# Optimization experiments

Hardware: AMD Instinct MI355X
Metric: run time of the kernel (lower is better)

## Reference

```python
import jax, jax.numpy as jnp
import numpy as np

EMBED_DIM = 1024
PROJ_DIM = 512
NUM_HEADS = 8
HEAD_DIM = PROJ_DIM // NUM_HEADS
B, L = 2, 2048


def setup_inputs() -> dict:
    key = jax.random.key(0)
    ks = jax.random.split(key, 7)
    s = lambda d: 1.0 / np.sqrt(d)
    return {
        "x": jax.random.normal(ks[0], (B, L, EMBED_DIM), jnp.float32),
        "proj_W": jax.random.normal(ks[1], (EMBED_DIM, PROJ_DIM), jnp.float32) * s(EMBED_DIM),
        "proj_b": jax.random.normal(ks[2], (PROJ_DIM,), jnp.float32) * 0.01,
        "attn_Wq": jax.random.normal(ks[3], (PROJ_DIM, NUM_HEADS, HEAD_DIM), jnp.float32) * s(PROJ_DIM),
        "attn_Wk": jax.random.normal(ks[4], (PROJ_DIM, NUM_HEADS, HEAD_DIM), jnp.float32) * s(PROJ_DIM),
        "attn_Wv": jax.random.normal(ks[5], (PROJ_DIM, NUM_HEADS, HEAD_DIM), jnp.float32) * s(PROJ_DIM),
        "out_W": jax.random.normal(ks[6], (NUM_HEADS * HEAD_DIM, EMBED_DIM), jnp.float32) * s(NUM_HEADS * HEAD_DIM),
    }


def reference(x, proj_W, proj_b, attn_Wq, attn_Wk, attn_Wv, out_W):
    # ReLU projection: (B, L, embed_dim) -> (B, L, proj_dim)
    p = jax.nn.relu(x @ proj_W + proj_b)
    # Per-head projections: (B, L, C) x (C, H, Dh) -> (B, H, L, Dh)
    q = jnp.einsum('blc,chd->bhld', p, attn_Wq)
    k = jnp.einsum('blc,chd->bhld', p, attn_Wk)
    v = jnp.einsum('blc,chd->bhld', p, attn_Wv)
    scale = 1.0 / np.sqrt(HEAD_DIM).astype(np.float32)
    scores = jnp.einsum('bhqd,bhkd->bhqk', q, k) * scale  # (B, H, L, L)
    weights = jax.nn.softmax(scores, axis=-1)
    heads = jnp.einsum('bhqk,bhkd->bhqd', weights, v)  # (B, H, L, Dh)
    heads = heads.transpose(0, 2, 1, 3).reshape(p.shape[0], p.shape[1], NUM_HEADS * HEAD_DIM)
    return heads @ out_W  # (B, L, embed_dim)
```

## Files before the change

kernel.cpp:

```cpp
#include <hip/hip_runtime.h>
#include <math.h>

#define BATCH 2
#define SEQ 2048
#define BL (BATCH * SEQ)
#define EMBED 1024
#define PROJ 512
#define NHEADS 8
#define HDIM 64
#define QKVN (3 * PROJ)
#define KVSPLIT 4
#define KVQ (SEQ / KVSPLIT)

typedef _Float16 half8 __attribute__((ext_vector_type(8)));
typedef __fp16 fp16x2 __attribute__((ext_vector_type(2)));
typedef float floatx4 __attribute__((ext_vector_type(4)));
typedef float floatx16 __attribute__((ext_vector_type(16)));

__global__ __launch_bounds__(256) void trconv_all(const float* __restrict__ pW,
                                                  const float* __restrict__ Wq,
                                                  const float* __restrict__ Wk,
                                                  const float* __restrict__ Wv,
                                                  const float* __restrict__ oW,
                                                  _Float16* __restrict__ pWt,
                                                  _Float16* __restrict__ qkvWt,
                                                  _Float16* __restrict__ oWt) {
    __shared__ float tile[64][65];
    int id = blockIdx.x;
    const float* src;
    _Float16* dst;
    int K, N;
    float scale = 1.0f;
    if (id < 128)      { src = pW; dst = pWt; K = EMBED; N = PROJ; }
    else if (id < 192) { src = Wq; dst = qkvWt; K = PROJ; N = PROJ;
                         scale = 0.125f * 1.44269504f; id -= 128; }
    else if (id < 256) { src = Wk; dst = qkvWt + (size_t)PROJ * PROJ; K = PROJ; N = PROJ; id -= 192; }
    else if (id < 320) { src = Wv; dst = qkvWt + (size_t)2 * PROJ * PROJ; K = PROJ; N = PROJ; id -= 256; }
    else               { src = oW; dst = oWt; K = PROJ; N = EMBED; id -= 320; }

    const int tn = N / 64;
    const int n0 = (id % tn) * 64;
    const int k0 = (id / tn) * 64;

    const int t  = threadIdx.x;
    const int tx = t & 63;
    const int ty = t >> 6;
#pragma unroll
    for (int i = 0; i < 16; ++i) {
        int k = ty * 16 + i;
        tile[k][tx] = src[(size_t)(k0 + k) * N + n0 + tx];
    }
    __syncthreads();
#pragma unroll
    for (int i = 0; i < 16; ++i) {
        int n = ty * 16 + i;
        dst[(size_t)(n0 + n) * K + k0 + tx] = (_Float16)(tile[tx][n] * scale);
    }
}

__global__ __launch_bounds__(256) void trans_v(const _Float16* __restrict__ v,
                                               _Float16* __restrict__ vt) {
    __shared__ _Float16 tile[64][72];
    const int t  = threadIdx.x;
    const int t0 = blockIdx.x * 64;
    const int h  = blockIdx.y;
    const int b  = blockIdx.z;
    {
        const int r = t >> 2, c0 = (t & 3) * 16;
        const _Float16* src = v + (size_t)(b * SEQ + t0 + r) * QKVN + h * HDIM + c0;
        *reinterpret_cast<half8*>(&tile[r][c0])     = *reinterpret_cast<const half8*>(src);
        *reinterpret_cast<half8*>(&tile[r][c0 + 8]) = *reinterpret_cast<const half8*>(src + 8);
    }
    __syncthreads();
    {
        const int c = t >> 2, k0 = (t & 3) * 16;
        half8 o1, o2;
#pragma unroll
        for (int i = 0; i < 8; ++i) { o1[i] = tile[k0 + i][c]; o2[i] = tile[k0 + 8 + i][c]; }
        _Float16* dst = vt + ((size_t)(b * NHEADS + h) * HDIM + c) * SEQ + t0 + k0;
        *reinterpret_cast<half8*>(dst)     = o1;
        *reinterpret_cast<half8*>(dst + 8) = o2;
    }
}

template <int BM, int BN, int A_F32, int BIASRELU, int C_F32>
__global__ __launch_bounds__(256) void gemm_mfma(const void* __restrict__ Ap,
                                                 const _Float16* __restrict__ Bt,
                                                 const float* __restrict__ bias,
                                                 void* __restrict__ Cp,
                                                 int M, int N, int K) {
    __shared__ _Float16 Ah[BM][40];
    __shared__ _Float16 Bh[BN][40];

    constexpr int MF = BM / 32;
    constexpr int NF = BN / 32;
    constexpr int EPA = BM / 8;
    constexpr int TPA = 32 / EPA;
    constexpr int EPB = BN / 8;
    constexpr int TPB = 32 / EPB;

    const int t  = threadIdx.x;
    const int w  = t >> 6;
    const int l  = t & 63;
    const int lr = l & 15;
    const int lg = l >> 4;
    const int bm = blockIdx.y * BM;
    const int bn = blockIdx.x * BN;
    const int wr = w >> 1;
    const int wc = w & 1;

    const int ar = t / TPA, ac = (t % TPA) * EPA;
    const int br = t / TPB, bc = (t % TPB) * EPB;

    floatx4 acc[MF][NF];
#pragma unroll
    for (int i = 0; i < MF; ++i)
#pragma unroll
        for (int j = 0; j < NF; ++j) acc[i][j] = (floatx4){0.f, 0.f, 0.f, 0.f};

    float4 af[EPA / 4];
    half8  ah[EPA / 8];
    half8  bh[EPB / 8];

    const float* Af = (const float*)Ap;
    const _Float16* Ah16 = (const _Float16*)Ap;

    if (A_F32) {
#pragma unroll
        for (int i = 0; i < EPA / 4; ++i)
            af[i] = *reinterpret_cast<const float4*>(&Af[(size_t)(bm + ar) * K + ac + i * 4]);
    } else {
#pragma unroll
        for (int i = 0; i < EPA / 8; ++i)
            ah[i] = *reinterpret_cast<const half8*>(&Ah16[(size_t)(bm + ar) * K + ac + i * 8]);
    }
#pragma unroll
    for (int i = 0; i < EPB / 8; ++i)
        bh[i] = *reinterpret_cast<const half8*>(&Bt[(size_t)(bn + br) * K + bc + i * 8]);

    for (int kt = 0; kt < K; kt += 32) {
        if (A_F32) {
#pragma unroll
            for (int i = 0; i < EPA / 8; ++i) {
                half8 hcv;
                float4 a0 = af[2 * i], a1 = af[2 * i + 1];
                hcv[0] = (_Float16)a0.x; hcv[1] = (_Float16)a0.y;
                hcv[2] = (_Float16)a0.z; hcv[3] = (_Float16)a0.w;
                hcv[4] = (_Float16)a1.x; hcv[5] = (_Float16)a1.y;
                hcv[6] = (_Float16)a1.z; hcv[7] = (_Float16)a1.w;
                *reinterpret_cast<half8*>(&Ah[ar][ac + i * 8]) = hcv;
            }
        } else {
#pragma unroll
            for (int i = 0; i < EPA / 8; ++i)
                *reinterpret_cast<half8*>(&Ah[ar][ac + i * 8]) = ah[i];
        }
#pragma unroll
        for (int i = 0; i < EPB / 8; ++i)
            *reinterpret_cast<half8*>(&Bh[br][bc + i * 8]) = bh[i];
        __syncthreads();

        if (kt + 32 < K) {
            if (A_F32) {
#pragma unroll
                for (int i = 0; i < EPA / 4; ++i)
                    af[i] = *reinterpret_cast<const float4*>(&Af[(size_t)(bm + ar) * K + kt + 32 + ac + i * 4]);
            } else {
#pragma unroll
                for (int i = 0; i < EPA / 8; ++i)
                    ah[i] = *reinterpret_cast<const half8*>(&Ah16[(size_t)(bm + ar) * K + kt + 32 + ac + i * 8]);
            }
#pragma unroll
            for (int i = 0; i < EPB / 8; ++i)
                bh[i] = *reinterpret_cast<const half8*>(&Bt[(size_t)(bn + br) * K + kt + 32 + bc + i * 8]);
        }

        half8 afr[MF], bfr[NF];
#pragma unroll
        for (int mf = 0; mf < MF; ++mf)
            afr[mf] = *reinterpret_cast<const half8*>(&Ah[wr * (BM / 2) + mf * 16 + lr][lg * 8]);
#pragma unroll
        for (int nf = 0; nf < NF; ++nf)
            bfr[nf] = *reinterpret_cast<const half8*>(&Bh[wc * (BN / 2) + nf * 16 + lr][lg * 8]);
        __builtin_amdgcn_s_setprio(1);
#pragma unroll
        for (int mf = 0; mf < MF; ++mf)
#pragma unroll
            for (int nf = 0; nf < NF; ++nf)
                acc[mf][nf] = __builtin_amdgcn_mfma_f32_16x16x32_f16(afr[mf], bfr[nf], acc[mf][nf], 0, 0, 0);
        __builtin_amdgcn_s_setprio(0);

        __syncthreads();
    }

#pragma unroll
    for (int mf = 0; mf < MF; ++mf)
#pragma unroll
        for (int nf = 0; nf < NF; ++nf) {
            const int n = bn + wc * (BN / 2) + nf * 16 + lr;
            float bs = 0.f;
            if (BIASRELU) bs = bias[n];
#pragma unroll
            for (int r = 0; r < 4; ++r) {
                const int m = bm + wr * (BM / 2) + mf * 16 + lg * 4 + r;
                float v = acc[mf][nf][r];
                if (BIASRELU) v = fmaxf(v + bs, 0.f);
                if (C_F32)
                    ((float*)Cp)[(size_t)m * N + n] = v;
                else
                    ((_Float16*)Cp)[(size_t)m * N + n] = (_Float16)v;
            }
        }
}

__global__ __launch_bounds__(256, 4) void attn_part(const _Float16* __restrict__ Q,
                                                    const _Float16* __restrict__ K,
                                                    const _Float16* __restrict__ Vt,
                                                    _Float16* __restrict__ Op,
                                                    float* __restrict__ ml) {
    __shared__ _Float16 Ks[2][64][64];
    __shared__ _Float16 Vs[2][64][64];
    __shared__ float Fs[4][32];

    const int t  = threadIdx.x;
    const int w  = t >> 6;
    const int l  = t & 63;
    const int ql = l & 31;
    const int hi = l >> 5;

    const int qt  = blockIdx.x >> 2;
    const int kvs = blockIdx.x & 3;
    const int q0  = qt * 128;
    const int h   = blockIdx.y;
    const int b   = blockIdx.z;
    const size_t base  = (size_t)b * SEQ * QKVN + (size_t)h * HDIM;
    const size_t vbase = (size_t)(b * NHEADS + h) * HDIM * SEQ;
    const size_t poff  = (((size_t)kvs * BATCH + b) * NHEADS + h) * SEQ;

    const int kt0  = kvs * KVQ;
    const int kend = kt0 + KVQ;

    half8 qf[4];
#pragma unroll
    for (int s = 0; s < 4; ++s)
        qf[s] = *reinterpret_cast<const half8*>(
            &Q[base + (size_t)(q0 + w * 32 + ql) * QKVN + s * 16 + hi * 8]);

    floatx16 o0 = (floatx16)0.f, o1 = (floatx16)0.f;
    float m_s = -1e30f, l_s = 0.f;

    const int rkv  = t >> 2;
    const int c8   = (t & 3) * 2;
    const int swz0 = (c8 ^ (rkv & 7)) * 8;
    const int swz1 = ((c8 + 1) ^ (rkv & 7)) * 8;

    half8 ka0, ka1, va0, va1;
    {
        const _Float16* kp = K + base + (size_t)(kt0 + rkv) * QKVN + c8 * 8;
        ka0 = *reinterpret_cast<const half8*>(kp);
        ka1 = *reinterpret_cast<const half8*>(kp + 8);
        const _Float16* vp = Vt + vbase + (size_t)rkv * SEQ + kt0 + c8 * 8;
        va0 = *reinterpret_cast<const half8*>(vp);
        va1 = *reinterpret_cast<const half8*>(vp + 8);
    }

    int p = 0;
    for (int kt = kt0; kt < kend; kt += 64) {
        *reinterpret_cast<half8*>(&Ks[p][rkv][swz0]) = ka0;
        *reinterpret_cast<half8*>(&Ks[p][rkv][swz1]) = ka1;
        *reinterpret_cast<half8*>(&Vs[p][rkv][swz0]) = va0;
        *reinterpret_cast<half8*>(&Vs[p][rkv][swz1]) = va1;
        __syncthreads();

        if (kt + 64 < kend) {
            const _Float16* kp = K + base + (size_t)(kt + 64 + rkv) * QKVN + c8 * 8;
            ka0 = *reinterpret_cast<const half8*>(kp);
            ka1 = *reinterpret_cast<const half8*>(kp + 8);
            const _Float16* vp = Vt + vbase + (size_t)rkv * SEQ + (kt + 64) + c8 * 8;
            va0 = *reinterpret_cast<const half8*>(vp);
            va1 = *reinterpret_cast<const half8*>(vp + 8);
        }

        floatx16 st0 = (floatx16)0.f, st1 = (floatx16)0.f;
        __builtin_amdgcn_s_setprio(1);
#pragma unroll
        for (int s = 0; s < 4; ++s) {
            const int c0 = ((2 * s + hi) ^ (ql & 7)) * 8;
            half8 kf0 = *reinterpret_cast<const half8*>(&Ks[p][ql][c0]);
            half8 kf1 = *reinterpret_cast<const half8*>(&Ks[p][32 + ql][c0]);
            st0 = __builtin_amdgcn_mfma_f32_32x32x16_f16(kf0, qf[s], st0, 0, 0, 0);
            st1 = __builtin_amdgcn_mfma_f32_32x32x16_f16(kf1, qf[s], st1, 0, 0, 0);
        }
        __builtin_amdgcn_s_setprio(0);

        float tm = st0[0];
#pragma unroll
        for (int i = 1; i < 16; ++i) tm = fmaxf(tm, st0[i]);
#pragma unroll
        for (int i = 0; i < 16; ++i) tm = fmaxf(tm, st1[i]);
        tm = fmaxf(tm, __shfl_xor(tm, 32));
        if (!__all(tm <= m_s + 8.f)) {
            float mn = fmaxf(m_s, tm);
            float fs = exp2f(m_s - mn);
            m_s = mn;
            l_s *= fs;
            if (hi == 0) Fs[w][ql] = fs;
#pragma unroll
            for (int r = 0; r < 16; ++r) {
                float f = Fs[w][(r & 3) + 8 * (r >> 2) + 4 * hi];
                o0[r] *= f;
                o1[r] *= f;
            }
        }
        float sum = 0.f;
#pragma unroll
        for (int i = 0; i < 16; ++i) { float pv = exp2f(st0[i] - m_s); st0[i] = pv; sum += pv; }
#pragma unroll
        for (int i = 0; i < 16; ++i) { float pv = exp2f(st1[i] - m_s); st1[i] = pv; sum += pv; }
        sum += __shfl_xor(sum, 32);
        l_s += sum;

        __builtin_amdgcn_s_setprio(1);
#pragma unroll
        for (int tt = 0; tt < 4; ++tt) {
            const int rb = (tt & 1) * 8;
            float v0, v1, v2, v3, v4, v5, v6, v7;
            if (tt < 2) {
                v0 = st0[rb + 0]; v1 = st0[rb + 1]; v2 = st0[rb + 2]; v3 = st0[rb + 3];
                v4 = st0[rb + 4]; v5 = st0[rb + 5]; v6 = st0[rb + 6]; v7 = st0[rb + 7];
            } else {
                v0 = st1[rb + 0]; v1 = st1[rb + 1]; v2 = st1[rb + 2]; v3 = st1[rb + 3];
                v4 = st1[rb + 4]; v5 = st1[rb + 5]; v6 = st1[rb + 6]; v7 = st1[rb + 7];
            }
            union U { fp16x2 h; unsigned u; };
            U ua0; ua0.h = __builtin_amdgcn_cvt_pkrtz(v0, v1);
            U ua1; ua1.h = __builtin_amdgcn_cvt_pkrtz(v2, v3);
            U ub0; ub0.h = __builtin_amdgcn_cvt_pkrtz(v4, v5);
            U ub1; ub1.h = __builtin_amdgcn_cvt_pkrtz(v6, v7);
            const unsigned pa0 = __shfl_xor(ua0.u, 32);
            const unsigned pa1 = __shfl_xor(ua1.u, 32);
            const unsigned pb0 = __shfl_xor(ub0.u, 32);
            const unsigned pb1 = __shfl_xor(ub1.u, 32);
            union A { unsigned u[4]; half8 h8; } pA;
            pA.u[0] = hi ? pb0 : ua0.u;
            pA.u[1] = hi ? pb1 : ua1.u;
            pA.u[2] = hi ? ub0.u : pa0;
            pA.u[3] = hi ? ub1.u : pa1;
            const int cv = 2 * tt + hi;
            {
                const int c0 = ((cv ^ (ql & 7))) * 8;
                half8 vb0 = *reinterpret_cast<const half8*>(&Vs[p][ql][c0]);
                half8 vb1 = *reinterpret_cast<const half8*>(&Vs[p][32 + ql][c0]);
                o0 = __builtin_amdgcn_mfma_f32_32x32x16_f16(pA.h8, vb0, o0, 0, 0, 0);
                o1 = __builtin_amdgcn_mfma_f32_32x32x16_f16(pA.h8, vb1, o1, 0, 0, 0);
            }
        }
        __builtin_amdgcn_s_setprio(0);

        p ^= 1;
    }

    __syncthreads();
    if (hi == 0) Fs[w][ql] = l_s;
#pragma unroll
    for (int r = 0; r < 16; ++r) {
        const int qp = (r & 3) + 8 * (r >> 2) + 4 * hi;
        const float inv = 1.0f / Fs[w][qp];
        const int qrow = q0 + w * 32 + qp;
        Op[(poff + qrow) * HDIM + ql]      = (_Float16)(o0[r] * inv);
        Op[(poff + qrow) * HDIM + 32 + ql] = (_Float16)(o1[r] * inv);
    }
    if (hi == 0) {
        const int qrow = q0 + w * 32 + ql;
        reinterpret_cast<float2*>(ml)[poff + qrow] = make_float2(m_s, l_s);
    }
}

__global__ __launch_bounds__(256) void attn_merge(const _Float16* __restrict__ Op,
                                                  const float* __restrict__ ml,
                                                  _Float16* __restrict__ hd) {
    const int t  = threadIdx.x;
    const int q  = blockIdx.x * 64 + (t >> 2);
    const int d0 = (t & 3) * 16;
    const int h  = blockIdx.y;
    const int b  = blockIdx.z;

    size_t offs[KVSPLIT];
    float2 mls[KVSPLIT];
#pragma unroll
    for (int s = 0; s < KVSPLIT; ++s) {
        offs[s] = (((size_t)s * BATCH + b) * NHEADS + h) * SEQ + q;
        mls[s] = reinterpret_cast<const float2*>(ml)[offs[s]];
    }
    float m = mls[0].x;
#pragma unroll
    for (int s = 1; s < KVSPLIT; ++s) m = fmaxf(m, mls[s].x);
    float wgt[KVSPLIT];
    float wsum = 0.f;
#pragma unroll
    for (int s = 0; s < KVSPLIT; ++s) {
        wgt[s] = mls[s].y * exp2f(mls[s].x - m);
        wsum += wgt[s];
    }
    float inv = 1.0f / wsum;

    float o[16] = {};
#pragma unroll
    for (int s = 0; s < KVSPLIT; ++s) {
        const _Float16* pp = Op + offs[s] * HDIM + d0;
        half8 a = *reinterpret_cast<const half8*>(pp);
        half8 c = *reinterpret_cast<const half8*>(pp + 8);
        float wv = wgt[s] * inv;
#pragma unroll
        for (int i = 0; i < 8; ++i) {
            o[i]     += wv * (float)a[i];
            o[8 + i] += wv * (float)c[i];
        }
    }
    half8 o0, o1;
#pragma unroll
    for (int i = 0; i < 8; ++i) { o0[i] = (_Float16)o[i]; o1[i] = (_Float16)o[8 + i]; }
    _Float16* dst = hd + (size_t)(b * SEQ + q) * PROJ + h * HDIM + d0;
    *reinterpret_cast<half8*>(dst)     = o0;
    *reinterpret_cast<half8*>(dst + 8) = o1;
}

extern "C" void kernel_launch(void* const* d_in, const int* in_sizes, int n_in,
                              void* d_out, int out_size, void* d_ws, size_t ws_size,
                              hipStream_t stream) {
    const float* x  = (const float*)d_in[0];
    const float* pW = (const float*)d_in[1];
    const float* pb = (const float*)d_in[2];
    const float* Wq = (const float*)d_in[3];
    const float* Wk = (const float*)d_in[4];
    const float* Wv = (const float*)d_in[5];
    const float* oW = (const float*)d_in[6];
    float* out = (float*)d_out;

    _Float16* ws    = (_Float16*)d_ws;
    _Float16* p_h   = ws;
    _Float16* qkv   = p_h + (size_t)BL * PROJ;
    _Float16* hd    = qkv + (size_t)BL * QKVN;
    _Float16* pWt   = hd + (size_t)BL * PROJ;
    _Float16* qkvWt = pWt + (size_t)PROJ * EMBED;
    _Float16* oWt   = qkvWt + (size_t)QKVN * PROJ;
    _Float16* vtb   = oWt + (size_t)EMBED * PROJ;
    _Float16* Oph   = vtb + (size_t)BATCH * NHEADS * HDIM * SEQ;
    float*    mlb   = (float*)(Oph + (size_t)KVSPLIT * BATCH * NHEADS * SEQ * HDIM);

    dim3 blk(256);

    trconv_all<<<dim3(448), blk, 0, stream>>>(pW, Wq, Wk, Wv, oW, pWt, qkvWt, oWt);

    gemm_mfma<64, 64, 1, 1, 0><<<dim3(PROJ / 64, BL / 64), blk, 0, stream>>>(
        (const void*)x, pWt, pb, (void*)p_h, BL, PROJ, EMBED);

    gemm_mfma<128, 64, 0, 0, 0><<<dim3(QKVN / 64, BL / 128), blk, 0, stream>>>(
        (const void*)p_h, qkvWt, nullptr, (void*)qkv, BL, QKVN, PROJ);

    trans_v<<<dim3(SEQ / 64, NHEADS, BATCH), blk, 0, stream>>>(qkv + 2 * PROJ, vtb);

    attn_part<<<dim3((SEQ / 128) * KVSPLIT, NHEADS, BATCH), blk, 0, stream>>>(
        qkv, qkv + PROJ, vtb, Oph, mlb);
    attn_merge<<<dim3(SEQ / 64, NHEADS, BATCH), blk, 0, stream>>>(Oph, mlb, hd);

    gemm_mfma<128, 64, 0, 0, 1><<<dim3(EMBED / 64, BL / 128), blk, 0, stream>>>(
        (const void*)hd, oWt, nullptr, (void*)out, BL, EMBED, PROJ);
}
```

Baseline: 107.7 us.

## Fuse split-KV attention merge into output projection GEMM A-tile load

Removes the separate attn_merge kernel and the hd intermediate buffer. The output GEMM now reads the four partial attention outputs and their (m,l) stats directly, combines them while staging A tiles into shared memory, then runs MFMA. This saves one launch and a global write and read of hd. In exchange, each of the 16 column blocks re-reads and re-merges all four partials, which multiplies Oph traffic and merge arithmetic. The row max in attn_part is also changed to a tree reduction to shorten the dependency chain.

```diff
diff --git a/kernel.cpp b/kernel.cpp
--- a/kernel.cpp
+++ b/kernel.cpp
@@ -213,6 +213,122 @@
         }
 }
 
+__global__ __launch_bounds__(256) void gemm_out_merge(const _Float16* __restrict__ Oph,
+                                                      const float* __restrict__ ml2,
+                                                      const _Float16* __restrict__ Bt,
+                                                      float* __restrict__ C) {
+    constexpr int BM = 128, BN = 64, MF = 4, NF = 2, K = PROJ;
+    __shared__ _Float16 Ah[BM][40];
+    __shared__ _Float16 Bh[BN][40];
+
+    const int t  = threadIdx.x;
+    const int w  = t >> 6;
+    const int l  = t & 63;
+    const int lr = l & 15;
+    const int lg = l >> 4;
+    const int bm = blockIdx.y * BM;
+    const int bn = blockIdx.x * BN;
+    const int wr = w >> 1;
+    const int wc = w & 1;
+
+    const int ar = t >> 1, ac = (t & 1) * 16;
+    const int br = t >> 2, bc = (t & 3) * 8;
+
+    const int m  = bm + ar;
+    const int bb = m >> 11;
+    const int q  = m & (SEQ - 1);
+    const size_t obase = (size_t)bb * NHEADS * SEQ + q;
+
+    floatx4 acc[MF][NF];
+#pragma unroll
+    for (int i = 0; i < MF; ++i)
+#pragma unroll
+        for (int j = 0; j < NF; ++j) acc[i][j] = (floatx4){0.f, 0.f, 0.f, 0.f};
+
+    half8  ahp[2][KVSPLIT];
+    float2 mlr[KVSPLIT];
+    half8  bh;
+
+    auto loadA = [&](int kt) {
+        const int h  = (kt + ac) >> 6;
+        const int d0 = (kt + ac) & 63;
+#pragma unroll
+        for (int s = 0; s < KVSPLIT; ++s) {
+            const size_t ro = (size_t)s * BATCH * NHEADS * SEQ + obase + (size_t)h * SEQ;
+            const _Float16* pp = Oph + ro * HDIM + d0;
+            ahp[0][s] = *reinterpret_cast<const half8*>(pp);
+            ahp[1][s] = *reinterpret_cast<const half8*>(pp + 8);
+            mlr[s] = reinterpret_cast<const float2*>(ml2)[ro];
+        }
+    };
+
+    loadA(0);
+    bh = *reinterpret_cast<const half8*>(&Bt[(size_t)(bn + br) * K + bc]);
+
+    for (int kt = 0; kt < K; kt += 32) {
+        {
+            float mm = fmaxf(fmaxf(mlr[0].x, mlr[1].x), fmaxf(mlr[2].x, mlr[3].x));
+            float wv[KVSPLIT], wsum = 0.f;
+#pragma unroll
+            for (int s = 0; s < KVSPLIT; ++s) {
+                wv[s] = mlr[s].y * exp2f(mlr[s].x - mm);
+                wsum += wv[s];
+            }
+            float inv = 1.0f / wsum;
+#pragma unroll
+            for (int s = 0; s < KVSPLIT; ++s) wv[s] *= inv;
+#pragma unroll
+            for (int ch = 0; ch < 2; ++ch) {
+                float o[8] = {};
+#pragma unroll
+                for (int s = 0; s < KVSPLIT; ++s)
+#pragma unroll
+                    for (int i = 0; i < 8; ++i) o[i] += wv[s] * (float)ahp[ch][s][i];
+                half8 hv;
+#pragma unroll
+                for (int i = 0; i < 8; ++i) hv[i] = (_Float16)o[i];
+                *reinterpret_cast<half8*>(&Ah[ar][ac + ch * 8]) = hv;
+            }
+        }
+        *reinterpret_cast<half8*>(&Bh[br][bc]) = bh;
+        __syncthreads();
+
+        if (kt + 32 < K) {
+            loadA(kt + 32);
+            bh = *reinterpret_cast<const half8*>(&Bt[(size_t)(bn + br) * K + kt + 32 + bc]);
+        }
+
+        half8 afr[MF], bfr[NF];
+#pragma unroll
+        for (int mf = 0; mf < MF; ++mf)
+            afr[mf] = *reinterpret_cast<const half8*>(&Ah[wr * 64 + mf * 16 + lr][lg * 8]);
+#pragma unroll
+        for (int nf = 0; nf < NF; ++nf)
+            bfr[nf] = *reinterpret_cast<const half8*>(&Bh[wc * 32 + nf * 16 + lr][lg * 8]);
+        __builtin_amdgcn_s_setprio(1);
+#pragma unroll
+        for (int mf = 0; mf < MF; ++mf)
+#pragma unroll
+            for (int nf = 0; nf < NF; ++nf)
+                acc[mf][nf] = __builtin_amdgcn_mfma_f32_16x16x32_f16(afr[mf], bfr[nf], acc[mf][nf], 0, 0, 0);
+        __builtin_amdgcn_s_setprio(0);
+
+        __syncthreads();
+    }
+
+#pragma unroll
+    for (int mf = 0; mf < MF; ++mf)
+#pragma unroll
+        for (int nf = 0; nf < NF; ++nf) {
+            const int n = bn + wc * 32 + nf * 16 + lr;
+#pragma unroll
+            for (int r = 0; r < 4; ++r) {
+                const int mm = bm + wr * 64 + mf * 16 + lg * 4 + r;
+                C[(size_t)mm * EMBED + n] = acc[mf][nf][r];
+            }
+        }
+}
+
 __global__ __launch_bounds__(256, 4) void attn_part(const _Float16* __restrict__ Q,
                                                     const _Float16* __restrict__ K,
                                                     const _Float16* __restrict__ Vt,
@@ -293,11 +409,14 @@
         }
         __builtin_amdgcn_s_setprio(0);
 
-        float tm = st0[0];
-#pragma unroll
-        for (int i = 1; i < 16; ++i) tm = fmaxf(tm, st0[i]);
-#pragma unroll
-        for (int i = 0; i < 16; ++i) tm = fmaxf(tm, st1[i]);
+        float mx[16];
+#pragma unroll
+        for (int i = 0; i < 16; ++i) mx[i] = fmaxf(st0[i], st1[i]);
+#pragma unroll
+        for (int i = 0; i < 8; ++i) mx[i] = fmaxf(mx[i], mx[i + 8]);
+#pragma unroll
+        for (int i = 0; i < 4; ++i) mx[i] = fmaxf(mx[i], mx[i + 4]);
+        float tm = fmaxf(fmaxf(mx[0], mx[1]), fmaxf(mx[2], mx[3]));
         tm = fmaxf(tm, __shfl_xor(tm, 32));
         if (!__all(tm <= m_s + 8.f)) {
             float mn = fmaxf(m_s, tm);
@@ -376,55 +495,6 @@
     }
 }
 
-__global__ __launch_bounds__(256) void attn_merge(const _Float16* __restrict__ Op,
-                                                  const float* __restrict__ ml,
-                                                  _Float16* __restrict__ hd) {
-    const int t  = threadIdx.x;
-    const int q  = blockIdx.x * 64 + (t >> 2);
-    const int d0 = (t & 3) * 16;
-    const int h  = blockIdx.y;
-    const int b  = blockIdx.z;
-
-    size_t offs[KVSPLIT];
-    float2 mls[KVSPLIT];
-#pragma unroll
-    for (int s = 0; s < KVSPLIT; ++s) {
-        offs[s] = (((size_t)s * BATCH + b) * NHEADS + h) * SEQ + q;
-        mls[s] = reinterpret_cast<const float2*>(ml)[offs[s]];
-    }
-    float m = mls[0].x;
-#pragma unroll
-    for (int s = 1; s < KVSPLIT; ++s) m = fmaxf(m, mls[s].x);
-    float wgt[KVSPLIT];
-    float wsum = 0.f;
-#pragma unroll
-    for (int s = 0; s < KVSPLIT; ++s) {
-        wgt[s] = mls[s].y * exp2f(mls[s].x - m);
-        wsum += wgt[s];
-    }
-    float inv = 1.0f / wsum;
-
-    float o[16] = {};
-#pragma unroll
-    for (int s = 0; s < KVSPLIT; ++s) {
-        const _Float16* pp = Op + offs[s] * HDIM + d0;
-        half8 a = *reinterpret_cast<const half8*>(pp);
-        half8 c = *reinterpret_cast<const half8*>(pp + 8);
-        float wv = wgt[s] * inv;
-#pragma unroll
-        for (int i = 0; i < 8; ++i) {
-            o[i]     += wv * (float)a[i];
-            o[8 + i] += wv * (float)c[i];
-        }
-    }
-    half8 o0, o1;
-#pragma unroll
-    for (int i = 0; i < 8; ++i) { o0[i] = (_Float16)o[i]; o1[i] = (_Float16)o[8 + i]; }
-    _Float16* dst = hd + (size_t)(b * SEQ + q) * PROJ + h * HDIM + d0;
-    *reinterpret_cast<half8*>(dst)     = o0;
-    *reinterpret_cast<half8*>(dst + 8) = o1;
-}
-
 extern "C" void kernel_launch(void* const* d_in, const int* in_sizes, int n_in,
                               void* d_out, int out_size, void* d_ws, size_t ws_size,
                               hipStream_t stream) {
@@ -440,8 +510,7 @@
     _Float16* ws    = (_Float16*)d_ws;
     _Float16* p_h   = ws;
     _Float16* qkv   = p_h + (size_t)BL * PROJ;
-    _Float16* hd    = qkv + (size_t)BL * QKVN;
-    _Float16* pWt   = hd + (size_t)BL * PROJ;
+    _Float16* pWt   = qkv + (size_t)BL * QKVN;
     _Float16* qkvWt = pWt + (size_t)PROJ * EMBED;
     _Float16* oWt   = qkvWt + (size_t)QKVN * PROJ;
     _Float16* vtb   = oWt + (size_t)EMBED * PROJ;
@@ -462,8 +531,7 @@
 
     attn_part<<<dim3((SEQ / 128) * KVSPLIT, NHEADS, BATCH), blk, 0, stream>>>(
         qkv, qkv + PROJ, vtb, Oph, mlb);
-    attn_merge<<<dim3(SEQ / 64, NHEADS, BATCH), blk, 0, stream>>>(Oph, mlb, hd);
-
-    gemm_mfma<128, 64, 0, 0, 1><<<dim3(EMBED / 64, BL / 128), blk, 0, stream>>>(
-        (const void*)hd, oWt, nullptr, (void*)out, BL, EMBED, PROJ);
+
+    gemm_out_merge<<<dim3(EMBED / 64, BL / 128), blk, 0, stream>>>(
+        Oph, mlb, oWt, out);
 }
```

Result: slower. 122.7 us (+14.0%).
